# Performance work log

Measured on AMD Instinct MI355X. Metric: run time of the kernel, lower is better.

The kernel has to match this reference:

```python
import jax, jax.numpy as jnp
import numpy as np

TEMPERATURE = 8.0  # sqrt(d_k=64)


def setup_inputs() -> dict:
    key = jax.random.key(0)
    ks = jax.random.split(key, 7)
    B, Lq, Lk, H, DK, DV, R, R2 = 4, 1024, 1024, 8, 64, 64, 32, 16
    return {
        "q":    jax.random.normal(ks[0], (B, Lq, H, DK), jnp.float32),
        "W_A":  jax.random.normal(ks[1], (H, DK, R),  jnp.float32) * 0.1,
        "W_B":  jax.random.normal(ks[2], (H, R, R2),  jnp.float32) * 0.1,
        "W_At": jax.random.normal(ks[3], (H, R, DK),  jnp.float32) * 0.1,
        "W_Bt": jax.random.normal(ks[4], (H, R2, R),  jnp.float32) * 0.1,
        "qt":   jax.random.normal(ks[5], (B, H, DK, Lk), jnp.float32),
        "v":    jax.random.normal(ks[6], (B, H, Lk, DV), jnp.float32),
        "d_k":  64,
        "mask": jnp.ones((B, 1, Lq, Lk), dtype=bool),
    }


def reference(q, W_A, W_B, W_At, W_Bt, qt, v, d_k, mask):
    # Low-rank projection chain: q -> A -> B -> Bt -> At  (per head b)
    IA      = jnp.einsum('kabc,bcd->kabd', q, W_A)        # [B,Lq,H,R]
    IAB     = jnp.einsum('kabj,bji->kabi', IA, W_B)       # [B,Lq,H,R2]
    IABBt   = jnp.einsum('kabi,bim->kabm', IAB, W_Bt)     # [B,Lq,H,R]
    IABBtAt = jnp.einsum('kabm,bmj->kabj', IABBt, W_At)   # [B,Lq,H,DK]
    # Bilinear score against transposed keys qt: [B,H,DK,Lk]
    attn = jnp.einsum('kabj,kbjm->kbam', IABBtAt, qt) / TEMPERATURE  # [B,H,Lq,Lk]
    attn = jnp.where(mask, attn, -1e9)
    attn = jax.nn.softmax(attn, axis=-1)
    # dropout p=0 (inference/reference) -> identity
    output = jnp.matmul(attn, v)  # [B,H,Lq,DV]
    return output, attn
```

## Files before the change

kernel.cpp:

```cpp
#include <hip/hip_runtime.h>

typedef short short8 __attribute__((ext_vector_type(8)));
typedef float f32x4 __attribute__((ext_vector_type(4)));

__device__ inline unsigned short f2bf(float f) {
    unsigned u = __builtin_bit_cast(unsigned, f);
    u += 0x7fff + ((u >> 16) & 1);
    return (unsigned short)(u >> 16);
}
__device__ inline short8 as_short8(uint4 v) { return __builtin_bit_cast(short8, v); }

__global__ void weff_kernel(const float* __restrict__ WA, const float* __restrict__ WB,
                            const float* __restrict__ WBt, const float* __restrict__ WAt,
                            float* __restrict__ Weff) {
    int h = blockIdx.x;
    int r = threadIdx.x;
    float wa[32];
#pragma unroll
    for (int c = 0; c < 32; ++c) wa[c] = WA[(h * 64 + r) * 32 + c];
    float t1[16];
#pragma unroll
    for (int i = 0; i < 16; ++i) {
        float s = 0.f;
#pragma unroll
        for (int c = 0; c < 32; ++c) s += wa[c] * WB[(h * 32 + c) * 16 + i];
        t1[i] = s;
    }
    float t2[32];
#pragma unroll
    for (int m = 0; m < 32; ++m) {
        float s = 0.f;
#pragma unroll
        for (int i = 0; i < 16; ++i) s += t1[i] * WBt[(h * 16 + i) * 32 + m];
        t2[m] = s;
    }
    for (int k = 0; k < 64; ++k) {
        float s = 0.f;
#pragma unroll
        for (int m = 0; m < 32; ++m) s += t2[m] * WAt[(h * 32 + m) * 64 + k];
        Weff[h * 4096 + r * 64 + k] = s;
    }
}

__global__ __launch_bounds__(256) void qp_kernel(const float* __restrict__ q,
                                                 const float* __restrict__ Weff,
                                                 unsigned short* __restrict__ Qp) {
    __shared__ float Wl[4096];
    __shared__ float qrow[4][64];
    int tid = threadIdx.x;
    int bh = blockIdx.x >> 8;
    int rb = (blockIdx.x & 255) * 4;
    int b = bh >> 3, h = bh & 7;
#pragma unroll
    for (int i = 0; i < 16; ++i) Wl[i * 256 + tid] = Weff[h * 4096 + i * 256 + tid];
    int rl = tid >> 6, k = tid & 63;
    qrow[rl][k] = q[((size_t)(b * 1024 + rb + rl) * 8 + h) * 64 + k];
    __syncthreads();
    float s = 0.f;
#pragma unroll
    for (int j = 0; j < 64; ++j) s += qrow[rl][j] * Wl[j * 64 + k];
    Qp[((size_t)bh * 1024 + rb + rl) * 64 + k] = f2bf(s * 0.125f);
}

__global__ __launch_bounds__(256) void repack_kernel(const float* __restrict__ qt,
                                                     const float* __restrict__ v,
                                                     uint4* __restrict__ qtp,
                                                     uint4* __restrict__ vp) {
    int g = blockIdx.x * 256 + threadIdx.x;
    int lane = g & 63;
    const float* src;
    uint4* dst;
    size_t jstride;
    if (g < 262144) {
        int kc = (g >> 6) & 1;
        int nt = (g >> 7) & 63;
        int bh = g >> 13;
        int k = kc * 32 + (lane >> 4) * 8;
        int n = nt * 16 + (lane & 15);
        src = qt + ((size_t)bh * 64 + k) * 1024 + n;
        jstride = 1024;
        dst = qtp + g;
    } else {
        int g2 = g - 262144;
        int kc = (g2 >> 6) & 31;
        int nt = (g2 >> 11) & 3;
        int bh = g2 >> 13;
        int k = kc * 32 + (lane >> 4) * 8;
        int n = nt * 16 + (lane & 15);
        src = v + ((size_t)bh * 1024 + k) * 64 + n;
        jstride = 64;
        dst = vp + g2;
    }
    unsigned short e[8];
#pragma unroll
    for (int j = 0; j < 8; ++j) e[j] = f2bf(src[jstride * j]);
    uint4 o;
    o.x = e[0] | ((unsigned)e[1] << 16);
    o.y = e[2] | ((unsigned)e[3] << 16);
    o.z = e[4] | ((unsigned)e[5] << 16);
    o.w = e[6] | ((unsigned)e[7] << 16);
    *dst = o;
}

__global__ __launch_bounds__(256, 4) void attn_kernel(
    const unsigned short* __restrict__ Qp,
    const uint4* __restrict__ qtp,
    const uint4* __restrict__ vp,
    float* __restrict__ outp,
    float* __restrict__ attnp) {
    constexpr int PST = 1032;
    __shared__ __align__(16) unsigned short Pbuf[16 * PST];
    __shared__ float redmax[4][16];
    __shared__ float redsum[4][16];

    const int tid = threadIdx.x;
    const int w = tid >> 6, lane = tid & 63;
    const int quad = lane >> 4, l16 = lane & 15;
    const int bh = blockIdx.x >> 6;
    const int mblk = blockIdx.x & 63;
    const int rowbase = bh * 1024 + mblk * 16;

    const uint4* qpb = (const uint4*)(Qp + ((size_t)(rowbase + l16)) * 64 + quad * 8);
    short8 a0 = as_short8(qpb[0]);
    short8 a1 = as_short8(qpb[4]);

    f32x4 acc[16];
    const uint4* qtb = qtp + (size_t)bh * 8192 + lane;
#pragma unroll
    for (int t = 0; t < 16; ++t) {
        int nt = w * 16 + t;
        uint4 b0 = qtb[(nt * 2 + 0) * 64];
        uint4 b1 = qtb[(nt * 2 + 1) * 64];
        f32x4 z = {0.f, 0.f, 0.f, 0.f};
        z = __builtin_amdgcn_mfma_f32_16x16x32_bf16(a0, as_short8(b0), z, 0, 0, 0);
        acc[t] = __builtin_amdgcn_mfma_f32_16x16x32_bf16(a1, as_short8(b1), z, 0, 0, 0);
    }

#pragma unroll
    for (int r = 0; r < 4; ++r) {
        float m = acc[0][r];
#pragma unroll
        for (int t = 1; t < 16; ++t) m = fmaxf(m, acc[t][r]);
#pragma unroll
        for (int off = 1; off < 16; off <<= 1) m = fmaxf(m, __shfl_xor(m, off, 64));
        if (l16 == 0) redmax[w][quad * 4 + r] = m;
    }
    __syncthreads();
    float rm[4];
#pragma unroll
    for (int r = 0; r < 4; ++r)
        rm[r] = fmaxf(fmaxf(redmax[0][quad * 4 + r], redmax[1][quad * 4 + r]),
                      fmaxf(redmax[2][quad * 4 + r], redmax[3][quad * 4 + r]));

    constexpr float LOG2E = 1.4426950408889634f;
    float sum[4] = {0.f, 0.f, 0.f, 0.f};
#pragma unroll
    for (int t = 0; t < 16; ++t) {
#pragma unroll
        for (int r = 0; r < 4; ++r) {
            float p = exp2f((acc[t][r] - rm[r]) * LOG2E);
            acc[t][r] = p;
            sum[r] += p;
        }
    }
#pragma unroll
    for (int r = 0; r < 4; ++r) {
#pragma unroll
        for (int off = 1; off < 16; off <<= 1) sum[r] += __shfl_xor(sum[r], off, 64);
        if (l16 == 0) redsum[w][quad * 4 + r] = sum[r];
    }
    __syncthreads();
    float inv[4];
#pragma unroll
    for (int r = 0; r < 4; ++r)
        inv[r] = 1.0f / (redsum[0][quad * 4 + r] + redsum[1][quad * 4 + r] +
                         redsum[2][quad * 4 + r] + redsum[3][quad * 4 + r]);

    float* abase = attnp + (size_t)rowbase * 1024 + w * 256 + l16;
#pragma unroll
    for (int t = 0; t < 16; ++t) {
#pragma unroll
        for (int r = 0; r < 4; ++r) {
            int rowl = quad * 4 + r;
            float p = acc[t][r] * inv[r];
            abase[rowl * 1024 + t * 16] = p;
            Pbuf[rowl * PST + w * 256 + t * 16 + l16] = f2bf(p);
        }
    }
    __syncthreads();

    f32x4 o = {0.f, 0.f, 0.f, 0.f};
    const uint4* vb = vp + (size_t)bh * 8192 + (size_t)w * 32 * 64 + lane;
    const unsigned short* prow = &Pbuf[l16 * PST + quad * 8];
#pragma unroll
    for (int kc = 0; kc < 32; ++kc) {
        short8 a = as_short8(*(const uint4*)(prow + kc * 32));
        uint4 b = vb[kc * 64];
        o = __builtin_amdgcn_mfma_f32_16x16x32_bf16(a, as_short8(b), o, 0, 0, 0);
    }
#pragma unroll
    for (int r = 0; r < 4; ++r)
        outp[((size_t)(rowbase + quad * 4 + r)) * 64 + w * 16 + l16] = o[r];
}

extern "C" void kernel_launch(void* const* d_in, const int* in_sizes, int n_in,
                              void* d_out, int out_size, void* d_ws, size_t ws_size,
                              hipStream_t stream) {
    (void)in_sizes; (void)n_in; (void)out_size; (void)ws_size;
    const float* q   = (const float*)d_in[0];
    const float* WA  = (const float*)d_in[1];
    const float* WB  = (const float*)d_in[2];
    const float* WAt = (const float*)d_in[3];
    const float* WBt = (const float*)d_in[4];
    const float* qt  = (const float*)d_in[5];
    const float* v   = (const float*)d_in[6];

    float* outp  = (float*)d_out;
    float* attnp = outp + (size_t)4 * 8 * 1024 * 64;

    char* ws = (char*)d_ws;
    float* Weff          = (float*)ws;
    unsigned short* Qp   = (unsigned short*)(ws + 131072);
    uint4* qtp           = (uint4*)(ws + 131072 + 4194304);
    uint4* vp            = (uint4*)(ws + 131072 + 2 * 4194304);

    hipLaunchKernelGGL(repack_kernel, dim3(2048), dim3(256), 0, stream, qt, v, qtp, vp);
    hipLaunchKernelGGL(weff_kernel, dim3(8), dim3(64), 0, stream, WA, WB, WBt, WAt, Weff);
    hipLaunchKernelGGL(qp_kernel, dim3(8192), dim3(256), 0, stream, q, Weff, Qp);
    hipLaunchKernelGGL(attn_kernel, dim3(2048), dim3(256), 0, stream, Qp, qtp, vp, outp, attnp);
}
```

Measured before the change: 251.0 us.

## Fuse repack and Q projection kernels, batch 16 rows per block, remap attn grid

Merges the qt/v bf16 repack kernel and the Q-projection kernel into one launch. Each Q-projection block now handles 16 rows instead of 4, so the 16KB Weff tile is reloaded into shared memory four times less often. The attention grid index is also remapped so that consecutive blocks cover different heads and batches rather than consecutive row blocks of the same head, which changes L2 reuse of the qtp and vp data. The fused kernel allocates the Wl shared memory for every block, including the repack blocks that do not use it, which may reduce their occupancy.

Result: no change. 248.6 us (-1.0%).

```diff
diff --git a/kernel.cpp b/kernel.cpp
--- a/kernel.cpp
+++ b/kernel.cpp
@@ -42,64 +42,74 @@
     }
 }
 
-__global__ __launch_bounds__(256) void qp_kernel(const float* __restrict__ q,
-                                                 const float* __restrict__ Weff,
-                                                 unsigned short* __restrict__ Qp) {
-    __shared__ float Wl[4096];
-    __shared__ float qrow[4][64];
-    int tid = threadIdx.x;
-    int bh = blockIdx.x >> 8;
-    int rb = (blockIdx.x & 255) * 4;
-    int b = bh >> 3, h = bh & 7;
-#pragma unroll
-    for (int i = 0; i < 16; ++i) Wl[i * 256 + tid] = Weff[h * 4096 + i * 256 + tid];
-    int rl = tid >> 6, k = tid & 63;
-    qrow[rl][k] = q[((size_t)(b * 1024 + rb + rl) * 8 + h) * 64 + k];
-    __syncthreads();
-    float s = 0.f;
-#pragma unroll
-    for (int j = 0; j < 64; ++j) s += qrow[rl][j] * Wl[j * 64 + k];
-    Qp[((size_t)bh * 1024 + rb + rl) * 64 + k] = f2bf(s * 0.125f);
-}
-
-__global__ __launch_bounds__(256) void repack_kernel(const float* __restrict__ qt,
-                                                     const float* __restrict__ v,
-                                                     uint4* __restrict__ qtp,
-                                                     uint4* __restrict__ vp) {
-    int g = blockIdx.x * 256 + threadIdx.x;
-    int lane = g & 63;
-    const float* src;
-    uint4* dst;
-    size_t jstride;
-    if (g < 262144) {
-        int kc = (g >> 6) & 1;
-        int nt = (g >> 7) & 63;
-        int bh = g >> 13;
-        int k = kc * 32 + (lane >> 4) * 8;
-        int n = nt * 16 + (lane & 15);
-        src = qt + ((size_t)bh * 64 + k) * 1024 + n;
-        jstride = 1024;
-        dst = qtp + g;
+__global__ __launch_bounds__(256) void pre_kernel(const float* __restrict__ qt,
+                                                  const float* __restrict__ v,
+                                                  const float* __restrict__ q,
+                                                  const float* __restrict__ Weff,
+                                                  uint4* __restrict__ qtp,
+                                                  uint4* __restrict__ vp,
+                                                  unsigned short* __restrict__ Qp) {
+    const int tid = threadIdx.x;
+    if (blockIdx.x < 2048) {
+        int g = blockIdx.x * 256 + tid;
+        int lane = g & 63;
+        const float* src;
+        uint4* dst;
+        size_t jstride;
+        if (g < 262144) {
+            int kc = (g >> 6) & 1;
+            int nt = (g >> 7) & 63;
+            int bh = g >> 13;
+            int k = kc * 32 + (lane >> 4) * 8;
+            int n = nt * 16 + (lane & 15);
+            src = qt + ((size_t)bh * 64 + k) * 1024 + n;
+            jstride = 1024;
+            dst = qtp + g;
+        } else {
+            int g2 = g - 262144;
+            int kc = (g2 >> 6) & 31;
+            int nt = (g2 >> 11) & 3;
+            int bh = g2 >> 13;
+            int k = kc * 32 + (lane >> 4) * 8;
+            int n = nt * 16 + (lane & 15);
+            src = v + ((size_t)bh * 1024 + k) * 64 + n;
+            jstride = 64;
+            dst = vp + g2;
+        }
+        unsigned short e[8];
+#pragma unroll
+        for (int j = 0; j < 8; ++j) e[j] = f2bf(src[jstride * j]);
+        uint4 o;
+        o.x = e[0] | ((unsigned)e[1] << 16);
+        o.y = e[2] | ((unsigned)e[3] << 16);
+        o.z = e[4] | ((unsigned)e[5] << 16);
+        o.w = e[6] | ((unsigned)e[7] << 16);
+        *dst = o;
     } else {
-        int g2 = g - 262144;
-        int kc = (g2 >> 6) & 31;
-        int nt = (g2 >> 11) & 3;
-        int bh = g2 >> 13;
-        int k = kc * 32 + (lane >> 4) * 8;
-        int n = nt * 16 + (lane & 15);
-        src = v + ((size_t)bh * 1024 + k) * 64 + n;
-        jstride = 64;
-        dst = vp + g2;
-    }
-    unsigned short e[8];
-#pragma unroll
-    for (int j = 0; j < 8; ++j) e[j] = f2bf(src[jstride * j]);
-    uint4 o;
-    o.x = e[0] | ((unsigned)e[1] << 16);
-    o.y = e[2] | ((unsigned)e[3] << 16);
-    o.z = e[4] | ((unsigned)e[5] << 16);
-    o.w = e[6] | ((unsigned)e[7] << 16);
-    *dst = o;
+        __shared__ float Wl[4096];
+        __shared__ float qrow[16][64];
+        int idx = blockIdx.x - 2048;
+        int bh = idx >> 6;
+        int rb = (idx & 63) * 16;
+        int b = bh >> 3, h = bh & 7;
+#pragma unroll
+        for (int i = 0; i < 16; ++i) Wl[i * 256 + tid] = Weff[h * 4096 + i * 256 + tid];
+        int rl = tid >> 6, k = tid & 63;
+#pragma unroll
+        for (int p = 0; p < 4; ++p) {
+            int row = p * 4 + rl;
+            qrow[row][k] = q[((size_t)(b * 1024 + rb + row) * 8 + h) * 64 + k];
+        }
+        __syncthreads();
+#pragma unroll
+        for (int p = 0; p < 4; ++p) {
+            int row = p * 4 + rl;
+            float s = 0.f;
+#pragma unroll
+            for (int j = 0; j < 64; ++j) s += qrow[row][j] * Wl[j * 64 + k];
+            Qp[((size_t)(bh * 1024 + rb + row)) * 64 + k] = f2bf(s * 0.125f);
+        }
+    }
 }
 
 __global__ __launch_bounds__(256, 4) void attn_kernel(
@@ -116,8 +126,8 @@
     const int tid = threadIdx.x;
     const int w = tid >> 6, lane = tid & 63;
     const int quad = lane >> 4, l16 = lane & 15;
-    const int bh = blockIdx.x >> 6;
-    const int mblk = blockIdx.x & 63;
+    const int bh = blockIdx.x & 31;
+    const int mblk = blockIdx.x >> 5;
     const int rowbase = bh * 1024 + mblk * 16;
 
     const uint4* qpb = (const uint4*)(Qp + ((size_t)(rowbase + l16)) * 64 + quad * 8);
@@ -224,8 +234,7 @@
     uint4* qtp           = (uint4*)(ws + 131072 + 4194304);
     uint4* vp            = (uint4*)(ws + 131072 + 2 * 4194304);
 
-    hipLaunchKernelGGL(repack_kernel, dim3(2048), dim3(256), 0, stream, qt, v, qtp, vp);
     hipLaunchKernelGGL(weff_kernel, dim3(8), dim3(64), 0, stream, WA, WB, WBt, WAt, Weff);
-    hipLaunchKernelGGL(qp_kernel, dim3(8192), dim3(256), 0, stream, q, Weff, Qp);
+    hipLaunchKernelGGL(pre_kernel, dim3(4096), dim3(256), 0, stream, qt, v, q, Weff, qtp, vp, Qp);
     hipLaunchKernelGGL(attn_kernel, dim3(2048), dim3(256), 0, stream, Qp, qtp, vp, outp, attnp);
 }
```
